# Kernel optimization log

Measured on AMD Instinct MI355X. Metric: run time of the kernel, lower is better.

## Reference

```python
import jax, jax.numpy as jnp
import numpy as np

M_FILT = 16      # number of dendrite filters m
CLASSES = 10
IMG = 96         # input image side
N = 9            # dendrite window side
B = 16           # batch
S = IMG - N + 1  # 88, sliding-window output side
SP = S // 4      # 22, after MaxPool3d((4,4,1))


def setup_inputs() -> dict:
    key = jax.random.key(0)
    ks = jax.random.split(key, 7)
    x = jax.random.normal(ks[0], (B, IMG, IMG), jnp.float32)
    w = jax.random.normal(ks[1], (M_FILT, N, N), jnp.float32)
    q = jax.random.normal(ks[2], (M_FILT, N, N), jnp.float32)
    fin = M_FILT * SP * SP
    fc1_w = jax.random.normal(ks[3], (128, fin), jnp.float32) / np.sqrt(fin).astype(np.float32)
    fc1_b = jax.random.normal(ks[4], (128,), jnp.float32) * 0.01
    fc2_w = jax.random.normal(ks[5], (CLASSES, 128), jnp.float32) / np.float32(np.sqrt(128.0))
    fc2_b = jax.random.normal(ks[6], (CLASSES,), jnp.float32) * 0.01
    return dict(x=x, w=w, q=q, fc1_w=fc1_w, fc1_b=fc1_b, fc2_w=fc2_w, fc2_b=fc2_b)


def _dendrite(x, w, q):
    # Faithful to torch: y = (pi + 2*atan(10*(x*w - q))) / (2*pi);
    # prod over window cols (dim 5), log, sum over window rows (dim 4).
    # Computed window-offset-by-window-offset to avoid materializing
    # the [B,S,S,m,N,N] tensor the torch code builds.
    b = x.shape[0]
    acc = jnp.zeros((b, S, S, M_FILT), x.dtype)
    for r in range(N):
        rowprod = jnp.ones((b, S, S, M_FILT), x.dtype)
        for c in range(N):
            xs = x[:, r:r + S, c:c + S][..., None]          # [B,S,S,1]
            t = (jnp.pi + 2.0 * jnp.arctan(10.0 * (xs * w[:, r, c] - q[:, r, c]))) / (2.0 * jnp.pi)
            rowprod = rowprod * (t + 0.6)                   # prod over cols
        acc = acc + jnp.log(rowprod)                        # log then sum over rows
    return acc  # [B,S,S,M_FILT]


def reference(x, w, q, fc1_w, fc1_b, fc2_w, fc2_b):
    y = _dendrite(x, w, q)                                  # [B,S,S,m]
    b = y.shape[0]
    # Soma: MaxPool3d((4,4,1)) over (S,S,m) dims (stride = kernel)
    y = y.reshape(b, SP, 4, SP, 4, M_FILT).max(axis=(2, 4))  # [B,SP,SP,m]
    # Axon: flatten + Linear(fin,128) + ReLU  (torch view keeps memory order)
    y = y.reshape(b, M_FILT * SP * SP)
    h = jnp.maximum(y @ fc1_w.T + fc1_b, 0.0)               # [B,128]
    # Synapse: Linear(128, classes)
    return h @ fc2_w.T + fc2_b                              # [B,classes]
```

## Files before the change

### kernel.cpp

```cpp
#include <hip/hip_runtime.h>

#define BATCH 16
#define IMG 96
#define NWIN 9
#define M_FILT 16
#define SP 22
#define FIN (M_FILT * SP * SP)
#define NPP (SP * SP)

__device__ __forceinline__ float dend_t(float z) {
    const float K0 =  0.3183026482f;
    const float K1 = -0.10587727f;
    const float K2 =  0.06160671f;
    const float K3 = -0.03706178f;
    const float K4 =  0.01676006f;
    float r   = __builtin_amdgcn_rcpf(z);
    bool  big = __builtin_fabsf(z) > 1.0f;
    float u   = big ? -r : z;
    float s   = u * u;
    float p   = fmaf(s, K4, K3);
    p = fmaf(s, p, K2);
    p = fmaf(s, p, K1);
    p = fmaf(s, p, K0);
    float sg  = __builtin_copysignf(0.5f, z);
    float c   = 1.1f + (big ? sg : 0.0f);
    return fmaf(u, p, c);
}

__global__ __launch_bounds__(256, 4) void dendrite_pool_kernel(
    const float* __restrict__ x,
    const float* __restrict__ w,
    const float* __restrict__ q,
    float* __restrict__ pooled)
{
    __shared__ float sw[M_FILT][NWIN][12];
    __shared__ float sq[M_FILT][NWIN][12];
    for (int i = threadIdx.x; i < M_FILT * NWIN * 12; i += 256) {
        int c  = i % 12;
        int mr = i / 12;
        float vw = 0.f, vq = 0.f;
        if (c < 9) {
            int src = mr * 9 + c;
            vw = 10.0f * w[src];
            vq = -10.0f * q[src];
        }
        ((float*)sw)[i] = vw;
        ((float*)sq)[i] = vq;
    }
    __syncthreads();

    int t    = blockIdx.x * 256 + threadIdx.x;
    int m    = t & 15;
    int di   = (t >> 4) & 3;
    int rest = t >> 6;
    int b    = rest / NPP;
    int pp   = rest - b * NPP;
    int pj   = pp % SP;
    int pi   = pp / SP;

    const float* xb = x + b * IMG * IMG + (pi * 4 + di) * IMG + pj * 4;

    float pr0 = 1.f, pr1 = 1.f, pr2 = 1.f, pr3 = 1.f;

    #pragma unroll 1
    for (int r = 0; r < NWIN; ++r) {
        const float4* xr = reinterpret_cast<const float4*>(xb + r * IMG);
        float4 A = xr[0], B4 = xr[1], C4 = xr[2];
        float xv[12] = {A.x,A.y,A.z,A.w, B4.x,B4.y,B4.z,B4.w, C4.x,C4.y,C4.z,C4.w};

        const float4* wrow = reinterpret_cast<const float4*>(&sw[m][r][0]);
        const float4* qrow = reinterpret_cast<const float4*>(&sq[m][r][0]);
        float4 W0 = wrow[0], W1 = wrow[1];
        float4 Q0 = qrow[0], Q1 = qrow[1];
        float wv[9] = {W0.x,W0.y,W0.z,W0.w, W1.x,W1.y,W1.z,W1.w, sw[m][r][8]};
        float qv[9] = {Q0.x,Q0.y,Q0.z,Q0.w, Q1.x,Q1.y,Q1.z,Q1.w, sq[m][r][8]};

        #pragma unroll
        for (int c = 0; c < 9; ++c) {
            pr0 *= dend_t(fmaf(xv[c + 0], wv[c], qv[c]));
            pr1 *= dend_t(fmaf(xv[c + 1], wv[c], qv[c]));
            pr2 *= dend_t(fmaf(xv[c + 2], wv[c], qv[c]));
            pr3 *= dend_t(fmaf(xv[c + 3], wv[c], qv[c]));
        }
    }

    float best = fmaxf(fmaxf(pr0, pr1), fmaxf(pr2, pr3));
    best = fmaxf(best, __shfl_xor(best, 16, 64));
    best = fmaxf(best, __shfl_xor(best, 32, 64));
    if (di == 0) {
        pooled[b * FIN + pp * 16 + m] = __builtin_amdgcn_logf(best) * 0.69314718056f;
    }
}

__global__ __launch_bounds__(256) void fc1_kernel(
    const float* __restrict__ pooled,
    const float* __restrict__ w1,
    const float* __restrict__ b1,
    float* __restrict__ h)
{
    int o = blockIdx.x;
    const float* wr = w1 + o * FIN;

    float acc[BATCH];
    #pragma unroll
    for (int b = 0; b < BATCH; ++b) acc[b] = 0.f;

    for (int f = threadIdx.x; f < FIN; f += 256) {
        float wv = wr[f];
        #pragma unroll
        for (int b = 0; b < BATCH; ++b)
            acc[b] = fmaf(pooled[b * FIN + f], wv, acc[b]);
    }

    #pragma unroll
    for (int b = 0; b < BATCH; ++b) {
        #pragma unroll
        for (int off = 32; off > 0; off >>= 1)
            acc[b] += __shfl_down(acc[b], off, 64);
    }

    __shared__ float red[4][BATCH];
    int wid = threadIdx.x >> 6, lane = threadIdx.x & 63;
    if (lane == 0) {
        #pragma unroll
        for (int b = 0; b < BATCH; ++b) red[wid][b] = acc[b];
    }
    __syncthreads();
    if (threadIdx.x < BATCH) {
        int b = threadIdx.x;
        float s_ = red[0][b] + red[1][b] + red[2][b] + red[3][b] + b1[o];
        h[b * 128 + o] = fmaxf(s_, 0.f);
    }
}

__global__ __launch_bounds__(192) void fc2_kernel(
    const float* __restrict__ h,
    const float* __restrict__ w2,
    const float* __restrict__ b2,
    float* __restrict__ out)
{
    int t = threadIdx.x;
    if (t >= BATCH * 10) return;
    int b = t / 10;
    int c = t - b * 10;
    const float* hb = h + b * 128;
    const float* wr = w2 + c * 128;
    float s = 0.0f;
    #pragma unroll 8
    for (int k = 0; k < 128; ++k) s += hb[k] * wr[k];
    out[t] = s + b2[c];
}

extern "C" void kernel_launch(void* const* d_in, const int* in_sizes, int n_in,
                              void* d_out, int out_size, void* d_ws, size_t ws_size,
                              hipStream_t stream)
{
    const float* x    = (const float*)d_in[0];
    const float* w    = (const float*)d_in[1];
    const float* q    = (const float*)d_in[2];
    const float* fc1w = (const float*)d_in[3];
    const float* fc1b = (const float*)d_in[4];
    const float* fc2w = (const float*)d_in[5];
    const float* fc2b = (const float*)d_in[6];
    float* out = (float*)d_out;

    float* pooled = (float*)d_ws;
    float* h      = pooled + BATCH * FIN;

    dendrite_pool_kernel<<<1936, 256, 0, stream>>>(x, w, q, pooled);
    fc1_kernel<<<128, 256, 0, stream>>>(pooled, fc1w, fc1b, h);
    fc2_kernel<<<1, 192, 0, stream>>>(h, fc2w, fc2b, out);
}
```

Measured before the change: 145.6 us.

## Use packed f32 math for dendrite transfer and remap blocks per filter

Rewrites the dendrite kernel so each block handles one (batch, filter, chunk) tile, with the filter's weights held in shared memory as interleaved (w,q) pairs. The polynomial arctan approximation and the running products now use v_pk_mul_f32/v_pk_fma_f32 to handle two window positions per instruction, aiming to cut VALU instruction count. The grid grows to 2048 blocks with clamped padding positions, so some threads do redundant work. Outputs are now written with a stride of 16 floats across threads, and the occupancy hint is dropped from launch bounds.

Result: faster. 141.3 us (-3.0%).

```diff
diff --git a/kernel.cpp b/kernel.cpp
--- a/kernel.cpp
+++ b/kernel.cpp
@@ -8,86 +8,103 @@
 #define FIN (M_FILT * SP * SP)
 #define NPP (SP * SP)
 
-__device__ __forceinline__ float dend_t(float z) {
-    const float K0 =  0.3183026482f;
-    const float K1 = -0.10587727f;
-    const float K2 =  0.06160671f;
-    const float K3 = -0.03706178f;
-    const float K4 =  0.01676006f;
-    float r   = __builtin_amdgcn_rcpf(z);
-    bool  big = __builtin_fabsf(z) > 1.0f;
-    float u   = big ? -r : z;
-    float s   = u * u;
-    float p   = fmaf(s, K4, K3);
-    p = fmaf(s, p, K2);
-    p = fmaf(s, p, K1);
-    p = fmaf(s, p, K0);
-    float sg  = __builtin_copysignf(0.5f, z);
-    float c   = 1.1f + (big ? sg : 0.0f);
-    return fmaf(u, p, c);
+typedef float f32x2 __attribute__((ext_vector_type(2)));
+typedef float f32x4 __attribute__((ext_vector_type(4)));
+
+__device__ __forceinline__ f32x2 pk_mul(f32x2 a, f32x2 b) {
+    f32x2 d;
+    asm("v_pk_mul_f32 %0, %1, %2" : "=v"(d) : "v"(a), "v"(b));
+    return d;
+}
+__device__ __forceinline__ f32x2 pk_fma(f32x2 a, f32x2 b, f32x2 c) {
+    f32x2 d;
+    asm("v_pk_fma_f32 %0, %1, %2, %3" : "=v"(d) : "v"(a), "v"(b), "v"(c));
+    return d;
 }
 
-__global__ __launch_bounds__(256, 4) void dendrite_pool_kernel(
+__device__ __forceinline__ f32x2 dend_t2(f32x2 z, f32x2 CK0, f32x2 CK1,
+                                         f32x2 CK2, f32x2 CK3, f32x2 CK4) {
+    float rx = __builtin_amdgcn_rcpf(z.x);
+    float ry = __builtin_amdgcn_rcpf(z.y);
+    bool bx = __builtin_fabsf(z.x) > 1.0f;
+    bool by = __builtin_fabsf(z.y) > 1.0f;
+    f32x2 u;
+    u.x = bx ? -rx : z.x;
+    u.y = by ? -ry : z.y;
+    f32x2 s = pk_mul(u, u);
+    f32x2 p = pk_fma(s, CK4, CK3);
+    p = pk_fma(s, p, CK2);
+    p = pk_fma(s, p, CK1);
+    p = pk_fma(s, p, CK0);
+    f32x2 c;
+    float sgx = __builtin_copysignf(0.5f, z.x);
+    float sgy = __builtin_copysignf(0.5f, z.y);
+    c.x = 1.1f + (bx ? sgx : 0.0f);
+    c.y = 1.1f + (by ? sgy : 0.0f);
+    return pk_fma(u, p, c);
+}
+
+__global__ __launch_bounds__(256) void dendrite_pool_kernel(
     const float* __restrict__ x,
     const float* __restrict__ w,
     const float* __restrict__ q,
     float* __restrict__ pooled)
 {
-    __shared__ float sw[M_FILT][NWIN][12];
-    __shared__ float sq[M_FILT][NWIN][12];
-    for (int i = threadIdx.x; i < M_FILT * NWIN * 12; i += 256) {
-        int c  = i % 12;
-        int mr = i / 12;
-        float vw = 0.f, vq = 0.f;
-        if (c < 9) {
-            int src = mr * 9 + c;
-            vw = 10.0f * w[src];
-            vq = -10.0f * q[src];
-        }
-        ((float*)sw)[i] = vw;
-        ((float*)sq)[i] = vq;
+    const int tid   = threadIdx.x;
+    const int chunk = blockIdx.x & 7;
+    const int m     = (blockIdx.x >> 3) & 15;
+    const int b     = blockIdx.x >> 7;
+
+    __shared__ f32x2 swq[NWIN * NWIN];
+    if (tid < NWIN * NWIN) {
+        float wv = w[m * 81 + tid];
+        float qv = q[m * 81 + tid];
+        f32x2 t; t.x = 10.0f * wv; t.y = -10.0f * qv;
+        swq[tid] = t;
     }
     __syncthreads();
 
-    int t    = blockIdx.x * 256 + threadIdx.x;
-    int m    = t & 15;
-    int di   = (t >> 4) & 3;
-    int rest = t >> 6;
-    int b    = rest / NPP;
-    int pp   = rest - b * NPP;
-    int pj   = pp % SP;
-    int pi   = pp / SP;
+    const int di  = tid & 3;
+    const int ppl = tid >> 2;
+    const int pp  = chunk * 64 + ppl;
+    const int ppc = pp < NPP ? pp : (NPP - 1);
+    const int pj  = ppc % SP;
+    const int pi  = ppc / SP;
 
     const float* xb = x + b * IMG * IMG + (pi * 4 + di) * IMG + pj * 4;
 
-    float pr0 = 1.f, pr1 = 1.f, pr2 = 1.f, pr3 = 1.f;
+    const f32x2 CK0 = { 0.3183026482f,  0.3183026482f};
+    const f32x2 CK1 = {-0.10587727f,   -0.10587727f};
+    const f32x2 CK2 = { 0.06160671f,    0.06160671f};
+    const f32x2 CK3 = {-0.03706178f,   -0.03706178f};
+    const f32x2 CK4 = { 0.01676006f,    0.01676006f};
+
+    f32x2 PA = {1.0f, 1.0f};
+    f32x2 PB = {1.0f, 1.0f};
 
     #pragma unroll 1
     for (int r = 0; r < NWIN; ++r) {
-        const float4* xr = reinterpret_cast<const float4*>(xb + r * IMG);
-        float4 A = xr[0], B4 = xr[1], C4 = xr[2];
-        float xv[12] = {A.x,A.y,A.z,A.w, B4.x,B4.y,B4.z,B4.w, C4.x,C4.y,C4.z,C4.w};
-
-        const float4* wrow = reinterpret_cast<const float4*>(&sw[m][r][0]);
-        const float4* qrow = reinterpret_cast<const float4*>(&sq[m][r][0]);
-        float4 W0 = wrow[0], W1 = wrow[1];
-        float4 Q0 = qrow[0], Q1 = qrow[1];
-        float wv[9] = {W0.x,W0.y,W0.z,W0.w, W1.x,W1.y,W1.z,W1.w, sw[m][r][8]};
-        float qv[9] = {Q0.x,Q0.y,Q0.z,Q0.w, Q1.x,Q1.y,Q1.z,Q1.w, sq[m][r][8]};
+        const f32x4* xr = reinterpret_cast<const f32x4*>(xb + r * IMG);
+        f32x4 X0 = xr[0], X1 = xr[1], X2 = xr[2];
+        float xv[12] = {X0.x,X0.y,X0.z,X0.w, X1.x,X1.y,X1.z,X1.w, X2.x,X2.y,X2.z,X2.w};
 
         #pragma unroll
         for (int c = 0; c < 9; ++c) {
-            pr0 *= dend_t(fmaf(xv[c + 0], wv[c], qv[c]));
-            pr1 *= dend_t(fmaf(xv[c + 1], wv[c], qv[c]));
-            pr2 *= dend_t(fmaf(xv[c + 2], wv[c], qv[c]));
-            pr3 *= dend_t(fmaf(xv[c + 3], wv[c], qv[c]));
+            f32x2 wq = swq[r * 9 + c];
+            f32x2 zA, zB;
+            zA.x = fmaf(xv[c + 0], wq.x, wq.y);
+            zA.y = fmaf(xv[c + 1], wq.x, wq.y);
+            zB.x = fmaf(xv[c + 2], wq.x, wq.y);
+            zB.y = fmaf(xv[c + 3], wq.x, wq.y);
+            PA = pk_mul(PA, dend_t2(zA, CK0, CK1, CK2, CK3, CK4));
+            PB = pk_mul(PB, dend_t2(zB, CK0, CK1, CK2, CK3, CK4));
         }
     }
 
-    float best = fmaxf(fmaxf(pr0, pr1), fmaxf(pr2, pr3));
-    best = fmaxf(best, __shfl_xor(best, 16, 64));
-    best = fmaxf(best, __shfl_xor(best, 32, 64));
-    if (di == 0) {
+    float best = fmaxf(fmaxf(PA.x, PA.y), fmaxf(PB.x, PB.y));
+    best = fmaxf(best, __shfl_xor(best, 1, 64));
+    best = fmaxf(best, __shfl_xor(best, 2, 64));
+    if (di == 0 && pp < NPP) {
         pooled[b * FIN + pp * 16 + m] = __builtin_amdgcn_logf(best) * 0.69314718056f;
     }
 }
@@ -167,7 +184,7 @@
     float* pooled = (float*)d_ws;
     float* h      = pooled + BATCH * FIN;
 
-    dendrite_pool_kernel<<<1936, 256, 0, stream>>>(x, w, q, pooled);
+    dendrite_pool_kernel<<<2048, 256, 0, stream>>>(x, w, q, pooled);
     fc1_kernel<<<128, 256, 0, stream>>>(pooled, fc1w, fc1b, h);
     fc2_kernel<<<1, 192, 0, stream>>>(h, fc2w, fc2b, out);
 }
```
